# Optimization experiments

Measured on AMD Instinct MI355X. Metric: run time of the kernel, lower is better.

## Reference

```python
import jax, jax.numpy as jnp
import numpy as np

N, E, H, NH, RBF_K = 512, 4096, 128, 8, 64
CUTOFF = 10.0
HH = H * NH  # 1024


def setup_inputs() -> dict:
    key = jax.random.key(0)
    ks = jax.random.split(key, 30)
    def lin_w(k, fan_in, fan_out):
        return jax.random.normal(k, (fan_in, fan_out), jnp.float32) * (fan_in ** -0.5)
    inp = {
        'atom_embs': jax.random.normal(ks[0], (N, H), jnp.float32),
        'pos': jax.random.normal(ks[1], (N, 3), jnp.float32),
        'edge_weight': jax.random.normal(ks[2], (E,), jnp.float32),
        'edge_indices': jax.random.randint(ks[3], (2, E), 0, N, jnp.int64),
        'Wq': lin_w(ks[4], H, HH),
        'Wk': lin_w(ks[5], H, HH),
        'Wv': lin_w(ks[6], H, HH),
        'li_w': lin_w(ks[7], H, H), 'li_b': jnp.zeros((H,), jnp.float32),
        'lj_w': lin_w(ks[8], H, H), 'lj_b': jnp.zeros((H,), jnp.float32),
        'el_w': lin_w(ks[9], 3 * H, HH), 'el_b': jnp.zeros((HH,), jnp.float32),
        'rl_w': lin_w(ks[10], RBF_K, HH), 'rl_b': jnp.zeros((HH,), jnp.float32),
        'ol_w': lin_w(ks[11], HH, H), 'ol_b': jnp.zeros((H,), jnp.float32),
        'ln_g': jnp.ones((H,), jnp.float32), 'ln_b': jnp.zeros((H,), jnp.float32),
        'f1_w': lin_w(ks[12], H, H), 'f1_b': jnp.zeros((H,), jnp.float32),
        'f2_w': lin_w(ks[13], H, H), 'f2_b': jnp.zeros((H,), jnp.float32),
        'f3_w': lin_w(ks[14], H, H), 'f3_b': jnp.zeros((H,), jnp.float32),
    }
    return inp


def _scatter_softmax_cols(logits, seg, num_segments):
    # softmax over columns of `logits` grouped by seg (column -> source node)
    lt = logits.T                                   # [E_cols, E_rows]
    m = jax.ops.segment_max(lt, seg, num_segments=num_segments)
    e = jnp.exp(lt - m[seg])
    s = jax.ops.segment_sum(e, seg, num_segments=num_segments)
    return (e / s[seg]).T


def _rbf(d):
    # d: [E, 1]. ExponentialRBF with softplus(softplus_inverse(x)) == x identities
    centers = jnp.linspace(1.0, np.exp(-CUTOFF).astype(np.float32), RBF_K)
    widths = np.float32((0.5 / ((1.0 - np.exp(-CUTOFF)) / RBF_K)) ** 2)
    x = d / CUTOFF
    x3 = x ** 3; x4 = x3 * x; x5 = x4 * x
    cut = jnp.where(x < 1, 1 - 6 * x5 + 15 * x4 - 10 * x3, jnp.zeros_like(x))
    return cut * jnp.exp(-widths * (jnp.exp(-d) - centers) ** 2)   # [E, K]


def reference(atom_embs, pos, edge_weight, edge_indices, Wq, Wk, Wv,
              li_w, li_b, lj_w, lj_b, el_w, el_b, rl_w, rl_b, ol_w, ol_b,
              ln_g, ln_b, f1_w, f1_b, f2_w, f2_b, f3_w, f3_b):
    src, tgt = edge_indices[0], edge_indices[1]
    ew = edge_weight[:, None]
    ai = atom_embs[tgt] + ew                      # atom_embs_i (+= edge_weight)
    aj = atom_embs[src] + ew                      # atom_embs_j (+= edge_weight)
    Q = ai @ Wq
    K = ai @ Wk
    V = ai @ Wv                                   # [E, HH]
    logits = (Q @ K.T) * (H ** -0.5)              # [E, E]
    prod = _scatter_softmax_cols(logits, src, N)  # scatter_softmax over edge_indices[0]
    hi = ai @ li_w + li_b
    hj = aj @ lj_w + lj_b
    edge_ij = jnp.concatenate([hi + hj, hi - hj, hi * hj], axis=-1)  # [E, 3H]
    d = jnp.linalg.norm(pos[tgt] - pos[src], axis=-1)[:, None]       # [E, 1]
    feats = edge_ij @ el_w + el_b + _rbf(d) @ rl_w + rl_b + V        # [E, HH]
    msg = (prod @ feats) @ ol_w + ol_b            # [E, H]
    agg = jax.ops.segment_sum(msg, tgt, num_segments=N)              # [N, H]

    def ln(x):
        mu = jnp.mean(x, -1, keepdims=True)
        var = jnp.var(x, -1, keepdims=True)
        return (x - mu) / jnp.sqrt(var + 1e-5) * ln_g + ln_b

    h = ln(agg)
    sp = jax.nn.softplus
    h = sp(sp(sp(h @ f1_w + f1_b) @ f2_w + f2_b) @ f3_w + f3_b)
    return ln(h)
```

## Files before the change

kernel.cpp:

```cpp
#include <hip/hip_runtime.h>
#include <math.h>

#define N_NODES 512
#define NE      4096
#define H       128
#define HH      1024
#define RBFK    64
#define KCAT    576

typedef __attribute__((ext_vector_type(8))) short bf16x8;
typedef __attribute__((ext_vector_type(4))) float f32x4;
typedef __attribute__((ext_vector_type(4))) short short4v;

__device__ __forceinline__ short f2bf(float x) {
    unsigned u = __builtin_bit_cast(unsigned, x);
    unsigned r = u + 0x7FFFu + ((u >> 16) & 1u);
    return (short)(r >> 16);
}
__device__ __forceinline__ float bf2f(short s) {
    return __builtin_bit_cast(float, ((unsigned)(unsigned short)s) << 16);
}

__device__ __forceinline__ void gload16(const short* g, short* l) {
    __builtin_amdgcn_global_load_lds(
        (const __attribute__((address_space(1))) void*)g,
        (__attribute__((address_space(3))) void*)l, 16, 0, 0);
}


__global__ __launch_bounds__(512) void k_scan(
    const int* __restrict__ ei,
    int* __restrict__ srcG, int* __restrict__ tgtG,
    int* __restrict__ segStart, int* __restrict__ segStartT,
    int* __restrict__ cursorS, int* __restrict__ cursorT, int* __restrict__ nsegp,
    float* __restrict__ cvec)
{
    __shared__ int hS[N_NODES], hT[N_NODES], sS[N_NODES], sT[N_NODES];
    __shared__ int flag;
    int t = threadIdx.x;
    if (t == 0) {
        int any = 0;
        for (int i = 1; i < 128; i += 2) any |= ei[i];
        flag = (any == 0);
    }
    hS[t] = 0; hT[t] = 0;
    if (t < H) cvec[t] = 0.0f;
    __syncthreads();
    int is64 = flag;
    for (int e = t; e < NE; e += 512) {
        int s = is64 ? ei[2 * e]          : ei[e];
        int g = is64 ? ei[2 * NE + 2 * e] : ei[NE + e];
        srcG[e] = s; tgtG[e] = g;
        atomicAdd(&hS[s], 1);
        atomicAdd(&hT[g], 1);
    }
    __syncthreads();
    int cs = hS[t], ct = hT[t];
    sS[t] = cs; sT[t] = ct;
    __syncthreads();
    for (int off = 1; off < N_NODES; off <<= 1) {
        int a = (t >= off) ? sS[t - off] : 0;
        int b = (t >= off) ? sT[t - off] : 0;
        __syncthreads();
        sS[t] += a; sT[t] += b;
        __syncthreads();
    }
    segStart[t + 1]  = sS[t];
    segStartT[t + 1] = sT[t];
    if (t == 0) { segStart[0] = 0; segStartT[0] = 0; }
    cursorS[t] = sS[t] - cs;
    cursorT[t] = sT[t] - ct;
    hS[t] = (cs > 0) ? 1 : 0;
    __syncthreads();
    for (int off = 256; off > 0; off >>= 1) {
        if (t < off) hS[t] += hS[t + off];
        __syncthreads();
    }
    if (t == 0) nsegp[0] = hS[0];
}

__global__ void k_scatter(const int* __restrict__ src, const int* __restrict__ tgt,
                          const float* __restrict__ ew,
                          int* __restrict__ cursorS, int* __restrict__ cursorT,
                          int* __restrict__ srcS, int* __restrict__ tgtS,
                          float* __restrict__ ewS, int* __restrict__ idxT) {
    int e = blockIdx.x * blockDim.x + threadIdx.x;
    if (e < NE) {
        int s = src[e], g = tgt[e];
        int p = atomicAdd(&cursorS[s], 1);
        srcS[p] = s; tgtS[p] = g; ewS[p] = ew[e];
        int q = atomicAdd(&cursorT[g], 1);
        idxT[q] = p;
    }
}

#define RA 524288
#define RB 589824
#define RBZ 65536
#define RQ 131072
#define RK 131072
#define RD 131072
#define RE 32768
#define RG 65536
#define RF 4096
#define RTOT (RA+RB+RBZ+RQ+RK+RD+RE+RG+RF)

__global__ void k_prep_all(
    const float* __restrict__ atom_embs, const float* __restrict__ pos,
    const int* __restrict__ srcS, const int* __restrict__ tgtS, const float* __restrict__ ewS,
    const float* __restrict__ Wq, const float* __restrict__ Wk, const float* __restrict__ Wv,
    const float* __restrict__ li_w, const float* __restrict__ lj_w,
    const float* __restrict__ el_w, const float* __restrict__ rl_w,
    const float* __restrict__ ol_w, const float* __restrict__ el_b, const float* __restrict__ rl_b,
    short* __restrict__ Acat, short* __restrict__ ajB, short* __restrict__ BcatT,
    short* __restrict__ WqB, short* __restrict__ WkB, short* __restrict__ olT,
    short* __restrict__ liT, short* __restrict__ ljT, short* __restrict__ embB,
    float* __restrict__ cvec)
{
    int idx = blockIdx.x * blockDim.x + threadIdx.x;
    if (idx < RA) {
        int p = idx >> 7, h = idx & 127;
        int s = srcS[p], t = tgtS[p];
        float ew = ewS[p];
        Acat[(size_t)p * KCAT + h] = f2bf(atom_embs[t * H + h] + ew);
        ajB[idx] = f2bf(atom_embs[s * H + h] + ew);
        if (h < RBFK) {
            float dx = pos[t * 3 + 0] - pos[s * 3 + 0];
            float dy = pos[t * 3 + 1] - pos[s * 3 + 1];
            float dz = pos[t * 3 + 2] - pos[s * 3 + 2];
            float d = sqrtf(dx * dx + dy * dy + dz * dz);
            float x = d * 0.1f;
            float cut = 0.0f;
            if (x < 1.0f) {
                float x3 = x * x * x, x4 = x3 * x, x5 = x4 * x;
                cut = 1.0f - 6.0f * x5 + 15.0f * x4 - 10.0f * x3;
            }
            float ck = 1.0f + (float)h * (-0.015872295239210119f);
            float tt = expf(-d) - ck;
            Acat[(size_t)p * KCAT + 512 + h] = f2bf(cut * expf(-1024.0929857f * tt * tt));
        }
        return;
    }
    idx -= RA;
    if (idx < RB) {
        int k = idx >> 10, n = idx & 1023;
        float v = (k < 128) ? Wv[k * HH + n]
                : (k < 512) ? el_w[(k - 128) * HH + n]
                            : rl_w[(k - 512) * HH + n];
        BcatT[idx] = f2bf(v);
        return;
    }
    idx -= RB;
    if (idx < RBZ) { BcatT[RB + idx] = 0; return; }
    idx -= RBZ;
    if (idx < RQ) { WqB[idx] = f2bf(Wq[idx]); return; }
    idx -= RQ;
    if (idx < RK) { WkB[idx] = f2bf(Wk[idx]); return; }
    idx -= RK;
    if (idx < RD) {
        int h = idx >> 10, n = idx & 1023;
        olT[idx] = f2bf(ol_w[n * H + h]);
        return;
    }
    idx -= RD;
    if (idx < RE) {
        int which = idx >> 14, r = idx & 16383;
        int n = r >> 7, k = r & 127;
        (which ? ljT : liT)[r] = f2bf((which ? lj_w : li_w)[k * H + n]);
        return;
    }
    idx -= RE;
    if (idx < RG) { embB[idx] = f2bf(atom_embs[idx]); return; }
    idx -= RG;
    if (idx < RF) {
        int h = idx & 127, chunk = idx >> 7;
        float acc = 0.0f;
        int n0 = chunk * 32;
        for (int n = n0; n < n0 + 32; n++)
            acc += (el_b[n] + rl_b[n]) * ol_w[n * H + h];
        atomicAdd(&cvec[h], acc);
    }
}

__device__ __forceinline__ void gemm_body(
    short* As, short* Bs,
    const short* __restrict__ A, int lda,
    const short* __restrict__ B, int ldb,
    void* __restrict__ Cp, int ldc,
    int kbeg, int kend, float alpha, const float* __restrict__ bias,
    long zoff_pitch, int out_mode, int row0, int col0)
{
    const int tid = threadIdx.x;
    const int wave = tid >> 6, lane = tid & 63;

    f32x4 acc[4][4];
#pragma unroll
    for (int i = 0; i < 4; i++)
#pragma unroll
        for (int j = 0; j < 4; j++) acc[i][j] = (f32x4){0.f, 0.f, 0.f, 0.f};

    const int m0 = (wave >> 1) * 64, n0 = (wave & 1) * 64;
    const int lr = lane >> 3;
    const int lc = (lane & 7) * 8;
    const int cl = lane & 15, quad = lane >> 4;

    for (int k0 = kbeg; k0 < kend; k0 += 64) {
#pragma unroll
        for (int i = 0; i < 4; i++) {
            int r = wave * 32 + i * 8;
            gload16(A + (size_t)(row0 + r + lr) * lda + k0 + lc, As + r * 64);
            gload16(B + (size_t)(col0 + r + lr) * ldb + k0 + lc, Bs + r * 64);
        }
        __syncthreads();
#pragma unroll
        for (int kk = 0; kk < 64; kk += 32) {
            bf16x8 af[4], bf[4];
            int ko = kk + quad * 8;
#pragma unroll
            for (int i = 0; i < 4; i++)
                af[i] = *(const bf16x8*)(As + (m0 + i * 16 + cl) * 64 + ko);
#pragma unroll
            for (int j = 0; j < 4; j++)
                bf[j] = *(const bf16x8*)(Bs + (n0 + j * 16 + cl) * 64 + ko);
#pragma unroll
            for (int i = 0; i < 4; i++)
#pragma unroll
                for (int j = 0; j < 4; j++)
                    acc[i][j] = __builtin_amdgcn_mfma_f32_16x16x32_bf16(af[i], bf[j], acc[i][j], 0, 0, 0);
        }
        __syncthreads();
    }

    if (out_mode == 1) {
        short* C = (short*)Cp;
#pragma unroll
        for (int i = 0; i < 4; i++)
#pragma unroll
            for (int j = 0; j < 4; j++) {
                int cc = col0 + n0 + j * 16 + cl;
                float bv = bias ? bias[cc] : 0.0f;
#pragma unroll
                for (int reg = 0; reg < 4; reg++) {
                    int rr = row0 + m0 + i * 16 + quad * 4 + reg;
                    C[(size_t)rr * ldc + cc] = f2bf(acc[i][j][reg] * alpha + bv);
                }
            }
    } else if (out_mode == 3) {
        short* C = (short*)Cp;
#pragma unroll
        for (int i = 0; i < 4; i++)
#pragma unroll
            for (int j = 0; j < 4; j++) {
                int cc = col0 + n0 + j * 16 + cl;
                int rr = row0 + m0 + i * 16 + quad * 4;
                short4v pack;
#pragma unroll
                for (int reg = 0; reg < 4; reg++) pack[reg] = f2bf(acc[i][j][reg] * alpha);
                *(short4v*)(C + (size_t)cc * ldc + rr) = pack;
            }
    } else {
        float* C = (float*)Cp + zoff_pitch;
#pragma unroll
        for (int i = 0; i < 4; i++)
#pragma unroll
            for (int j = 0; j < 4; j++) {
                int cc = col0 + n0 + j * 16 + cl;
#pragma unroll
                for (int reg = 0; reg < 4; reg++) {
                    int rr = row0 + m0 + i * 16 + quad * 4 + reg;
                    C[(size_t)rr * ldc + cc] = acc[i][j][reg] * alpha;
                }
            }
    }
}

__global__ __launch_bounds__(256) void k_gemm(
    const short* __restrict__ A, int lda,
    const short* __restrict__ B, int ldb,
    void* __restrict__ Cp, int ldc,
    int K, float alpha, const float* __restrict__ bias,
    long split_pitch, int out_mode)
{
    __shared__ __align__(16) short As[128 * 64];
    __shared__ __align__(16) short Bs[128 * 64];
    int kchunk = K / gridDim.z;
    gemm_body(As, Bs, A, lda, B, ldb, Cp, ldc,
              kchunk * blockIdx.z, kchunk * (blockIdx.z + 1), alpha, bias,
              (long)blockIdx.z * split_pitch, out_mode,
              blockIdx.y * 128, blockIdx.x * 128);
}

__global__ __launch_bounds__(256) void k_smallgemms(
    const short* __restrict__ olT, const short* __restrict__ BcatT,
    const short* __restrict__ WqB, const short* __restrict__ WkB,
    short* __restrict__ W2T, short* __restrict__ MT)
{
    __shared__ __align__(16) short As[128 * 64];
    __shared__ __align__(16) short Bs[128 * 64];
    if (blockIdx.x < 5) {
        gemm_body(As, Bs, olT, HH, BcatT, HH, W2T, 640, 0, HH, 1.0f, nullptr, 0, 1,
                  0, blockIdx.x * 128);
    } else {
        gemm_body(As, Bs, WqB, HH, WkB, HH, MT, 128, 0, HH, 1.0f, nullptr, 0, 3, 0, 0);
    }
}

__global__ __launch_bounds__(256) void k_midgemms(
    const short* __restrict__ Acat, const short* __restrict__ W2T,
    const short* __restrict__ MT, const short* __restrict__ embB,
    short* __restrict__ GT, short* __restrict__ Y)
{
    __shared__ __align__(16) short As[128 * 64];
    __shared__ __align__(16) short Bs[128 * 64];
    if (blockIdx.x < 32) {
        gemm_body(As, Bs, Acat, KCAT, W2T, 640, GT, NE, 0, KCAT, 1.0f, nullptr, 0, 3,
                  blockIdx.x * 128, 0);
    } else {
        gemm_body(As, Bs, embB, H, MT, H, Y, H, 0, H, 1.0f, nullptr, 0, 1,
                  (blockIdx.x - 32) * 128, 0);
    }
}

__global__ __launch_bounds__(256) void k_zgemm(
    const short* __restrict__ Y, const short* __restrict__ embB,
    const short* __restrict__ MT, const int* __restrict__ tgtS,
    const float* __restrict__ ewS,
    float* __restrict__ Z, float* __restrict__ pv,
    float* __restrict__ colP, float* __restrict__ colB)
{
    const float alpha = 0.08838834764831845f;
    __shared__ __align__(16) short As[128 * 64];
    __shared__ __align__(16) short Bs[128 * 64];
    if (blockIdx.x < 16) {
        gemm_body(As, Bs, Y, H, embB, H, Z, N_NODES, 0, H, alpha, nullptr, 0, 0,
                  (blockIdx.x >> 2) * 128, (blockIdx.x & 3) * 128);
    } else {
        __shared__ float csM[H];
        __shared__ float qsh[N_NODES];
        __shared__ float sSh;
        int t = threadIdx.x;
        if (t < H) {
            float a = 0.0f;
            for (int i = 0; i < H; i++) a += bf2f(MT[t * H + i]);
            csM[t] = a;
        }
        __syncthreads();
        for (int n = t; n < N_NODES; n += 256) {
            float a = 0.0f, b = 0.0f;
            for (int k = 0; k < H; k++) {
                a += bf2f(Y[n * H + k]);
                b += csM[k] * bf2f(embB[n * H + k]);
            }
            pv[n] = a; qsh[n] = b;
        }
        if (t == 0) {
            float s = 0.0f;
            for (int k = 0; k < H; k++) s += csM[k];
            sSh = s;
        }
        __syncthreads();
        float s = sSh;
        for (int c = t; c < NE; c += 256) {
            float ec = ewS[c];
            colP[c] = alpha * ec;
            colB[c] = alpha * (qsh[tgtS[c]] + ec * s);
        }
    }
}

__global__ __launch_bounds__(256) void k_edgefeat(
    const short* __restrict__ Acat_in, const short* __restrict__ ajB,
    const short* __restrict__ liT, const short* __restrict__ ljT,
    const float* __restrict__ li_b, const float* __restrict__ lj_b,
    short* __restrict__ Acat)
{
    __shared__ __align__(16) short As[128 * 128];
    __shared__ __align__(16) short Bs[128 * 128];
    const int tid = threadIdx.x;
    const int wave = tid >> 6, lane = tid & 63;
    const int row0 = blockIdx.x * 128;
    const int cl = lane & 15, quad = lane >> 4;
    const int m0 = (wave >> 1) * 64, n0 = (wave & 1) * 64;
    const int sr = lane >> 4, sc = (lane & 15) * 8;

    f32x4 ai_acc[4][4], aj_acc[4][4];
#pragma unroll
    for (int i = 0; i < 4; i++)
#pragma unroll
        for (int j = 0; j < 4; j++) {
            ai_acc[i][j] = (f32x4){0.f, 0.f, 0.f, 0.f};
            aj_acc[i][j] = (f32x4){0.f, 0.f, 0.f, 0.f};
        }

#pragma unroll
    for (int i = 0; i < 8; i++) {
        int r = wave * 32 + i * 4;
        gload16(Acat_in + (size_t)(row0 + r + sr) * KCAT + sc, As + r * 128);
        gload16(liT + (r + sr) * 128 + sc, Bs + r * 128);
    }
    __syncthreads();
#pragma unroll
    for (int kk = 0; kk < 128; kk += 32) {
        bf16x8 af[4], bf[4];
        int ko = kk + quad * 8;
#pragma unroll
        for (int i = 0; i < 4; i++) af[i] = *(const bf16x8*)(As + (m0 + i * 16 + cl) * 128 + ko);
#pragma unroll
        for (int j = 0; j < 4; j++) bf[j] = *(const bf16x8*)(Bs + (n0 + j * 16 + cl) * 128 + ko);
#pragma unroll
        for (int i = 0; i < 4; i++)
#pragma unroll
            for (int j = 0; j < 4; j++)
                ai_acc[i][j] = __builtin_amdgcn_mfma_f32_16x16x32_bf16(af[i], bf[j], ai_acc[i][j], 0, 0, 0);
    }
    __syncthreads();
#pragma unroll
    for (int i = 0; i < 8; i++) {
        int r = wave * 32 + i * 4;
        gload16(ajB + (size_t)(row0 + r + sr) * 128 + sc, As + r * 128);
        gload16(ljT + (r + sr) * 128 + sc, Bs + r * 128);
    }
    __syncthreads();
#pragma unroll
    for (int kk = 0; kk < 128; kk += 32) {
        bf16x8 af[4], bf[4];
        int ko = kk + quad * 8;
#pragma unroll
        for (int i = 0; i < 4; i++) af[i] = *(const bf16x8*)(As + (m0 + i * 16 + cl) * 128 + ko);
#pragma unroll
        for (int j = 0; j < 4; j++) bf[j] = *(const bf16x8*)(Bs + (n0 + j * 16 + cl) * 128 + ko);
#pragma unroll
        for (int i = 0; i < 4; i++)
#pragma unroll
            for (int j = 0; j < 4; j++)
                aj_acc[i][j] = __builtin_amdgcn_mfma_f32_16x16x32_bf16(af[i], bf[j], aj_acc[i][j], 0, 0, 0);
    }
#pragma unroll
    for (int i = 0; i < 4; i++)
#pragma unroll
        for (int j = 0; j < 4; j++) {
            int cc = n0 + j * 16 + cl;
            float bi = li_b[cc], bj = lj_b[cc];
#pragma unroll
            for (int reg = 0; reg < 4; reg++) {
                int rr = row0 + m0 + i * 16 + quad * 4 + reg;
                float hv = ai_acc[i][j][reg] + bi;
                float gv = aj_acc[i][j][reg] + bj;
                short* rowp = Acat + (size_t)rr * KCAT;
                rowp[128 + cc] = f2bf(hv + gv);
                rowp[256 + cc] = f2bf(hv - gv);
                rowp[384 + cc] = f2bf(hv * gv);
            }
        }
}

__global__ __launch_bounds__(256) void k_softmax_z(
    const float* __restrict__ Z, const float* __restrict__ pv,
    const float* __restrict__ colP, const float* __restrict__ colB,
    const int* __restrict__ tgtS, const float* __restrict__ ewS,
    const int* __restrict__ srcS, const int* __restrict__ segStart,
    short* __restrict__ P)
{
    __shared__ float row[NE];
    __shared__ float zrow[N_NODES];
    __shared__ float rD[N_NODES];
    const int r = blockIdx.x, t = threadIdx.x;
    const int tr = tgtS[r];
    const float er = ewS[r];
    for (int i = t; i < N_NODES; i += 256)
        zrow[i] = Z[(size_t)tr * N_NODES + i];
    __syncthreads();
    const float p_tr = pv[tr];
    for (int c = t; c < NE; c += 256)
        row[c] = __expf(zrow[tgtS[c]] + colP[c] * p_tr + er * colB[c]);
    __syncthreads();
    for (int n = t; n < N_NODES; n += 256) {
        int a = segStart[n], b = segStart[n + 1];
        float s = 0.0f;
        for (int p = a; p < b; p++) s += row[p];
        rD[n] = (s > 0.0f) ? 1.0f / s : 0.0f;
    }
    __syncthreads();
    short* pr = P + (size_t)r * NE;
    for (int c = 2 * t; c < NE; c += 512) {
        unsigned lo = (unsigned short)f2bf(row[c] * rD[srcS[c]]);
        unsigned hi = (unsigned short)f2bf(row[c + 1] * rD[srcS[c + 1]]);
        *(unsigned*)(pr + c) = lo | (hi << 16);
    }
}

__global__ __launch_bounds__(128) void k_head(
    const float* __restrict__ msgP, const int* __restrict__ idxT,
    const int* __restrict__ segStartT, const int* __restrict__ nsegp,
    const float* __restrict__ cvec, const float* __restrict__ ol_b,
    const float* __restrict__ ln_g, const float* __restrict__ ln_b,
    const float* __restrict__ f1_w, const float* __restrict__ f1_b,
    const float* __restrict__ f2_w, const float* __restrict__ f2_b,
    const float* __restrict__ f3_w, const float* __restrict__ f3_b,
    float* __restrict__ out)
{
    __shared__ float x[H];
    __shared__ float red[H];
    int t = threadIdx.x, row = blockIdx.x;
    int a = segStartT[row], b = segStartT[row + 1];
    float v = (float)(b - a) * (ol_b[t] + (float)nsegp[0] * cvec[t]);
    for (int p = a; p < b; p++) {
        int e = idxT[p];
        const float* mp = msgP + (size_t)e * H + t;
#pragma unroll
        for (int z = 0; z < 4; z++) v += mp[(size_t)z * NE * H];
    }
    red[t] = v; __syncthreads();
    for (int s = 64; s > 0; s >>= 1) { if (t < s) red[t] += red[t + s]; __syncthreads(); }
    float mu = red[0] * (1.0f / H); __syncthreads();
    float dv = v - mu;
    red[t] = dv * dv; __syncthreads();
    for (int s = 64; s > 0; s >>= 1) { if (t < s) red[t] += red[t + s]; __syncthreads(); }
    float var = red[0] * (1.0f / H); __syncthreads();
    x[t] = dv * rsqrtf(var + 1e-5f) * ln_g[t] + ln_b[t];
    __syncthreads();
    const float* Ws[3] = { f1_w, f2_w, f3_w };
    const float* Bb[3] = { f1_b, f2_b, f3_b };
    for (int l = 0; l < 3; l++) {
        float acc = Bb[l][t];
        const float* Wl = Ws[l];
        for (int k = 0; k < H; k++) acc = fmaf(x[k], Wl[k * H + t], acc);
        float o = fmaxf(acc, 0.0f) + log1pf(expf(-fabsf(acc)));
        __syncthreads();
        x[t] = o;
        __syncthreads();
    }
    float xv = x[t];
    red[t] = xv; __syncthreads();
    for (int s = 64; s > 0; s >>= 1) { if (t < s) red[t] += red[t + s]; __syncthreads(); }
    mu = red[0] * (1.0f / H); __syncthreads();
    float dv2 = xv - mu;
    red[t] = dv2 * dv2; __syncthreads();
    for (int s = 64; s > 0; s >>= 1) { if (t < s) red[t] += red[t + s]; __syncthreads(); }
    var = red[0] * (1.0f / H);
    out[row * H + t] = dv2 * rsqrtf(var + 1e-5f) * ln_g[t] + ln_b[t];
}


extern "C" void kernel_launch(void* const* d_in, const int* in_sizes, int n_in,
                              void* d_out, int out_size, void* d_ws, size_t ws_size,
                              hipStream_t stream) {
    const float* atom_embs   = (const float*)d_in[0];
    const float* pos         = (const float*)d_in[1];
    const float* edge_weight = (const float*)d_in[2];
    const int*   edge_idx    = (const int*)d_in[3];
    const float* Wq   = (const float*)d_in[4];
    const float* Wk   = (const float*)d_in[5];
    const float* Wv   = (const float*)d_in[6];
    const float* li_w = (const float*)d_in[7];
    const float* li_b = (const float*)d_in[8];
    const float* lj_w = (const float*)d_in[9];
    const float* lj_b = (const float*)d_in[10];
    const float* el_w = (const float*)d_in[11];
    const float* el_b = (const float*)d_in[12];
    const float* rl_w = (const float*)d_in[13];
    const float* rl_b = (const float*)d_in[14];
    const float* ol_w = (const float*)d_in[15];
    const float* ol_b = (const float*)d_in[16];
    const float* ln_g = (const float*)d_in[17];
    const float* ln_b = (const float*)d_in[18];
    const float* f1_w = (const float*)d_in[19];
    const float* f1_b = (const float*)d_in[20];
    const float* f2_w = (const float*)d_in[21];
    const float* f2_b = (const float*)d_in[22];
    const float* f3_w = (const float*)d_in[23];
    const float* f3_b = (const float*)d_in[24];
    float* out = (float*)d_out;

    char* w = (char*)d_ws;
    size_t off = 0;
    auto alloc = [&](size_t bytes) -> void* {
        void* p = w + off;
        off += (bytes + 255) & ~(size_t)255;
        return p;
    };
    int*   src       = (int*)alloc(NE * 4);
    int*   tgt       = (int*)alloc(NE * 4);
    int*   srcS      = (int*)alloc(NE * 4);
    int*   tgtS      = (int*)alloc(NE * 4);
    float* ewS       = (float*)alloc(NE * 4);
    int*   segStart  = (int*)alloc((N_NODES + 1) * 4);
    int*   segStartT = (int*)alloc((N_NODES + 1) * 4);
    int*   cursorS   = (int*)alloc(N_NODES * 4);
    int*   cursorT   = (int*)alloc(N_NODES * 4);
    int*   idxT      = (int*)alloc(NE * 4);
    int*   nsegp     = (int*)alloc(4);
    short* Acat   = (short*)alloc((size_t)NE * KCAT * 2);
    short* ajB    = (short*)alloc((size_t)NE * H * 2);
    short* BcatT  = (short*)alloc((size_t)640 * HH * 2);
    short* WqB    = (short*)alloc((size_t)H * HH * 2);
    short* WkB    = (short*)alloc((size_t)H * HH * 2);
    short* olT    = (short*)alloc((size_t)H * HH * 2);
    short* liT    = (short*)alloc((size_t)H * H * 2);
    short* ljT    = (short*)alloc((size_t)H * H * 2);
    short* embB   = (short*)alloc((size_t)N_NODES * H * 2);
    float* cvec   = (float*)alloc(H * 4);
    short* W2T    = (short*)alloc((size_t)H * 640 * 2);
    short* MT     = (short*)alloc((size_t)H * H * 2);
    short* Y      = (short*)alloc((size_t)N_NODES * H * 2);
    float* Z      = (float*)alloc((size_t)N_NODES * N_NODES * 4);
    float* pv     = (float*)alloc(N_NODES * 4);
    float* colP   = (float*)alloc(NE * 4);
    float* colB   = (float*)alloc(NE * 4);
    short* GT     = (short*)alloc((size_t)H * NE * 2);
    short* prodB  = (short*)alloc((size_t)NE * NE * 2);
    float* msgP   = (float*)alloc((size_t)4 * NE * H * 4);

    k_scan<<<1, 512, 0, stream>>>(edge_idx, src, tgt, segStart, segStartT,
                                  cursorS, cursorT, nsegp, cvec);
    k_scatter<<<NE / 256, 256, 0, stream>>>(src, tgt, edge_weight, cursorS, cursorT,
                                            srcS, tgtS, ewS, idxT);
    k_prep_all<<<(RTOT + 255) / 256, 256, 0, stream>>>(
        atom_embs, pos, srcS, tgtS, ewS,
        Wq, Wk, Wv, li_w, lj_w, el_w, rl_w, ol_w, el_b, rl_b,
        Acat, ajB, BcatT, WqB, WkB, olT, liT, ljT, embB, cvec);
    k_edgefeat<<<NE / 128, 256, 0, stream>>>(Acat, ajB, liT, ljT, li_b, lj_b, Acat);

    k_smallgemms<<<6, 256, 0, stream>>>(olT, BcatT, WqB, WkB, W2T, MT);
    k_midgemms<<<36, 256, 0, stream>>>(Acat, W2T, MT, embB, GT, Y);
    k_zgemm<<<17, 256, 0, stream>>>(Y, embB, MT, tgtS, ewS, Z, pv, colP, colB);

    k_softmax_z<<<NE, 256, 0, stream>>>(Z, pv, colP, colB, tgtS, ewS, srcS, segStart, prodB);
    {
        dim3 g(1, NE / 128, 4);
        k_gemm<<<g, 256, 0, stream>>>(prodB, NE, GT, NE, msgP, H, NE, 1.0f, nullptr,
                                      (long)NE * H, 0);
    }
    k_head<<<N_NODES, H, 0, stream>>>(msgP, idxT, segStartT, nsegp, cvec, ol_b,
                                      ln_g, ln_b, f1_w, f1_b, f2_w, f2_b, f3_w, f3_b, out);
}
```

Baseline: 251.7 us.

## Fuse softmax probability generation into message GEMM, chunked by source segments

Removes the full E×E bf16 probability matrix. The softmax kernel now only writes per-row reciprocal denominators for each source segment. A new GEMM kernel rebuilds the probabilities on the fly from Z, colP/colB and those denominators while forming the A operand. Columns are split into chunks of 64 source nodes, so each block only iterates the columns of its segments, with partial sums reduced in the head kernel. This avoids a large HBM write and read. The cost is per-element exp and scattered gathers inside the GEMM loop, an extra denominator buffer, and a fixed width cap (MAXW) per chunk that silently truncates if a chunk holds too many edges.

```diff
diff --git a/kernel.cpp b/kernel.cpp
--- a/kernel.cpp
+++ b/kernel.cpp
@@ -7,6 +7,10 @@
 #define HH      1024
 #define RBFK    64
 #define KCAT    576
+#define GTLD    (NE + 128)
+#define NCHUNK  8
+#define SEGPC   64
+#define MAXW    768
 
 typedef __attribute__((ext_vector_type(8))) short bf16x8;
 typedef __attribute__((ext_vector_type(4))) float f32x4;
@@ -102,8 +106,9 @@
 #define RD 131072
 #define RE 32768
 #define RG 65536
+#define RGZ 16384
 #define RF 4096
-#define RTOT (RA+RB+RBZ+RQ+RK+RD+RE+RG+RF)
+#define RTOT (RA+RB+RBZ+RQ+RK+RD+RE+RG+RGZ+RF)
 
 __global__ void k_prep_all(
     const float* __restrict__ atom_embs, const float* __restrict__ pos,
@@ -115,7 +120,7 @@
     short* __restrict__ Acat, short* __restrict__ ajB, short* __restrict__ BcatT,
     short* __restrict__ WqB, short* __restrict__ WkB, short* __restrict__ olT,
     short* __restrict__ liT, short* __restrict__ ljT, short* __restrict__ embB,
-    float* __restrict__ cvec)
+    short* __restrict__ GT, float* __restrict__ cvec)
 {
     int idx = blockIdx.x * blockDim.x + threadIdx.x;
     if (idx < RA) {
@@ -172,6 +177,12 @@
     idx -= RE;
     if (idx < RG) { embB[idx] = f2bf(atom_embs[idx]); return; }
     idx -= RG;
+    if (idx < RGZ) {
+        int h = idx >> 7, t = idx & 127;
+        GT[(size_t)h * GTLD + NE + t] = 0;
+        return;
+    }
+    idx -= RGZ;
     if (idx < RF) {
         int h = idx & 127, chunk = idx >> 7;
         float acc = 0.0f;
@@ -274,22 +285,6 @@
     }
 }
 
-__global__ __launch_bounds__(256) void k_gemm(
-    const short* __restrict__ A, int lda,
-    const short* __restrict__ B, int ldb,
-    void* __restrict__ Cp, int ldc,
-    int K, float alpha, const float* __restrict__ bias,
-    long split_pitch, int out_mode)
-{
-    __shared__ __align__(16) short As[128 * 64];
-    __shared__ __align__(16) short Bs[128 * 64];
-    int kchunk = K / gridDim.z;
-    gemm_body(As, Bs, A, lda, B, ldb, Cp, ldc,
-              kchunk * blockIdx.z, kchunk * (blockIdx.z + 1), alpha, bias,
-              (long)blockIdx.z * split_pitch, out_mode,
-              blockIdx.y * 128, blockIdx.x * 128);
-}
-
 __global__ __launch_bounds__(256) void k_smallgemms(
     const short* __restrict__ olT, const short* __restrict__ BcatT,
     const short* __restrict__ WqB, const short* __restrict__ WkB,
@@ -313,7 +308,7 @@
     __shared__ __align__(16) short As[128 * 64];
     __shared__ __align__(16) short Bs[128 * 64];
     if (blockIdx.x < 32) {
-        gemm_body(As, Bs, Acat, KCAT, W2T, 640, GT, NE, 0, KCAT, 1.0f, nullptr, 0, 3,
+        gemm_body(As, Bs, Acat, KCAT, W2T, 640, GT, GTLD, 0, KCAT, 1.0f, nullptr, 0, 3,
                   blockIdx.x * 128, 0);
     } else {
         gemm_body(As, Bs, embB, H, MT, H, Y, H, 0, H, 1.0f, nullptr, 0, 1,
@@ -454,16 +449,14 @@
         }
 }
 
-__global__ __launch_bounds__(256) void k_softmax_z(
+__global__ __launch_bounds__(256) void k_denom(
     const float* __restrict__ Z, const float* __restrict__ pv,
     const float* __restrict__ colP, const float* __restrict__ colB,
     const int* __restrict__ tgtS, const float* __restrict__ ewS,
-    const int* __restrict__ srcS, const int* __restrict__ segStart,
-    short* __restrict__ P)
+    const int* __restrict__ segStart, float* __restrict__ rDen)
 {
     __shared__ float row[NE];
     __shared__ float zrow[N_NODES];
-    __shared__ float rD[N_NODES];
     const int r = blockIdx.x, t = threadIdx.x;
     const int tr = tgtS[r];
     const float er = ewS[r];
@@ -474,19 +467,128 @@
     for (int c = t; c < NE; c += 256)
         row[c] = __expf(zrow[tgtS[c]] + colP[c] * p_tr + er * colB[c]);
     __syncthreads();
+    float* rd = rDen + (size_t)r * N_NODES;
     for (int n = t; n < N_NODES; n += 256) {
         int a = segStart[n], b = segStart[n + 1];
         float s = 0.0f;
         for (int p = a; p < b; p++) s += row[p];
-        rD[n] = (s > 0.0f) ? 1.0f / s : 0.0f;
-    }
-    __syncthreads();
-    short* pr = P + (size_t)r * NE;
-    for (int c = 2 * t; c < NE; c += 512) {
-        unsigned lo = (unsigned short)f2bf(row[c] * rD[srcS[c]]);
-        unsigned hi = (unsigned short)f2bf(row[c + 1] * rD[srcS[c + 1]]);
-        *(unsigned*)(pr + c) = lo | (hi << 16);
-    }
+        rd[n] = (s > 0.0f) ? 1.0f / s : 0.0f;
+    }
+}
+
+__global__ __launch_bounds__(256) void k_msg(
+    const float* __restrict__ Z, const float* __restrict__ pv,
+    const float* __restrict__ colP, const float* __restrict__ colB,
+    const float* __restrict__ rDen,
+    const int* __restrict__ tgtS, const float* __restrict__ ewS,
+    const int* __restrict__ srcS, const int* __restrict__ segStart,
+    const short* __restrict__ GT, float* __restrict__ msgP)
+{
+    __shared__ float cP[MAXW], cB[MAXW];
+    __shared__ int   tcc[MAXW], sgc[MAXW];
+    __shared__ int   trOff[128];
+    __shared__ float ewrS[128], ptrS[128];
+    __shared__ __align__(16) short Bs[128 * 64];
+
+    const int tid = threadIdx.x;
+    const int bj = blockIdx.x;
+    const int r0 = blockIdx.y * 128;
+
+    const int cb = segStart[SEGPC * bj];
+    const int ce = segStart[SEGPC * bj + SEGPC];
+    const int cbase = cb & ~7;
+    int nk = (ce - cbase + 63) >> 6;
+    if (nk > MAXW / 64) nk = MAXW / 64;
+    const int wpad = nk << 6;
+
+    for (int lc = tid; lc < wpad; lc += 256) {
+        int c = cbase + lc;
+        if (c >= cb && c < ce) {
+            tcc[lc] = tgtS[c];
+            cP[lc]  = colP[c];
+            cB[lc]  = colB[c];
+            sgc[lc] = srcS[c];
+        } else sgc[lc] = -1;
+    }
+    if (tid < 128) {
+        int rr = r0 + tid;
+        int tr = tgtS[rr];
+        trOff[tid] = tr * N_NODES;
+        ewrS[tid] = ewS[rr];
+        ptrS[tid] = pv[tr];
+    }
+    __syncthreads();
+
+    const int wave = tid >> 6, lane = tid & 63;
+    const int m0 = (wave >> 1) * 64, n0 = (wave & 1) * 64;
+    const int lr = lane >> 3, lc8 = (lane & 7) * 8;
+    const int cl = lane & 15, quad = lane >> 4;
+
+    int zb4[4], rb4[4]; float pw4[4], er4[4];
+#pragma unroll
+    for (int i = 0; i < 4; i++) {
+        int m = m0 + i * 16 + cl;
+        zb4[i] = trOff[m]; pw4[i] = ptrS[m]; er4[i] = ewrS[m];
+        rb4[i] = (r0 + m) * N_NODES;
+    }
+
+    f32x4 acc[4][4];
+#pragma unroll
+    for (int i = 0; i < 4; i++)
+#pragma unroll
+        for (int j = 0; j < 4; j++) acc[i][j] = (f32x4){0.f, 0.f, 0.f, 0.f};
+
+    for (int k0 = 0; k0 < wpad; k0 += 64) {
+#pragma unroll
+        for (int i = 0; i < 4; i++) {
+            int hr = wave * 32 + i * 8;
+            gload16(GT + (size_t)(hr + lr) * GTLD + cbase + k0 + lc8, Bs + hr * 64);
+        }
+        __syncthreads();
+#pragma unroll
+        for (int kk = 0; kk < 64; kk += 32) {
+            bf16x8 bf[4];
+#pragma unroll
+            for (int j = 0; j < 4; j++)
+                bf[j] = *(const bf16x8*)(Bs + (n0 + j * 16 + cl) * 64 + kk + quad * 8);
+            bf16x8 af[4];
+#pragma unroll
+            for (int jj = 0; jj < 8; jj++) {
+                int lc = k0 + kk + quad * 8 + jj;
+                int sg = sgc[lc];
+                float cp = cP[lc], cbv = cB[lc];
+                int tc = (sg >= 0) ? tcc[lc] : 0;
+#pragma unroll
+                for (int i = 0; i < 4; i++) {
+                    float v = 0.0f;
+                    if (sg >= 0) {
+                        float l = Z[zb4[i] + tc] + cp * pw4[i] + er4[i] * cbv;
+                        v = __expf(l) * rDen[rb4[i] + sg];
+                    }
+                    af[i][jj] = f2bf(v);
+                }
+            }
+#pragma unroll
+            for (int i = 0; i < 4; i++)
+#pragma unroll
+                for (int j = 0; j < 4; j++)
+                    acc[i][j] = __builtin_amdgcn_mfma_f32_16x16x32_bf16(af[i], bf[j], acc[i][j], 0, 0, 0);
+        }
+        __syncthreads();
+    }
+
+    float* C = msgP + (size_t)bj * NE * H;
+#pragma unroll
+    for (int i = 0; i < 4; i++)
+#pragma unroll
+        for (int j = 0; j < 4; j++) {
+            int cc = n0 + j * 16 + cl;
+#pragma unroll
+            for (int reg = 0; reg < 4; reg++) {
+                int rr = r0 + m0 + i * 16 + quad * 4 + reg;
+                C[(size_t)rr * H + cc] = acc[i][j][reg];
+            }
+        }
 }
 
 __global__ __launch_bounds__(128) void k_head(
@@ -508,7 +610,7 @@
         int e = idxT[p];
         const float* mp = msgP + (size_t)e * H + t;
 #pragma unroll
-        for (int z = 0; z < 4; z++) v += mp[(size_t)z * NE * H];
+        for (int z = 0; z < NCHUNK; z++) v += mp[(size_t)z * NE * H];
     }
     red[t] = v; __syncthreads();
     for (int s = 64; s > 0; s >>= 1) { if (t < s) red[t] += red[t + s]; __syncthreads(); }
@@ -607,9 +709,9 @@
     float* pv     = (float*)alloc(N_NODES * 4);
     float* colP   = (float*)alloc(NE * 4);
     float* colB   = (float*)alloc(NE * 4);
-    short* GT     = (short*)alloc((size_t)H * NE * 2);
-    short* prodB  = (short*)alloc((size_t)NE * NE * 2);
-    float* msgP   = (float*)alloc((size_t)4 * NE * H * 4);
+    short* GT     = (short*)alloc((size_t)H * GTLD * 2);
+    float* rDen   = (float*)alloc((size_t)NE * N_NODES * 4);
+    float* msgP   = (float*)alloc((size_t)NCHUNK * NE * H * 4);
 
     k_scan<<<1, 512, 0, stream>>>(edge_idx, src, tgt, segStart, segStartT,
                                   cursorS, cursorT, nsegp, cvec);
@@ -618,18 +720,18 @@
     k_prep_all<<<(RTOT + 255) / 256, 256, 0, stream>>>(
         atom_embs, pos, srcS, tgtS, ewS,
         Wq, Wk, Wv, li_w, lj_w, el_w, rl_w, ol_w, el_b, rl_b,
-        Acat, ajB, BcatT, WqB, WkB, olT, liT, ljT, embB, cvec);
+        Acat, ajB, BcatT, WqB, WkB, olT, liT, ljT, embB, GT, cvec);
     k_edgefeat<<<NE / 128, 256, 0, stream>>>(Acat, ajB, liT, ljT, li_b, lj_b, Acat);
 
     k_smallgemms<<<6, 256, 0, stream>>>(olT, BcatT, WqB, WkB, W2T, MT);
     k_midgemms<<<36, 256, 0, stream>>>(Acat, W2T, MT, embB, GT, Y);
     k_zgemm<<<17, 256, 0, stream>>>(Y, embB, MT, tgtS, ewS, Z, pv, colP, colB);
 
-    k_softmax_z<<<NE, 256, 0, stream>>>(Z, pv, colP, colB, tgtS, ewS, srcS, segStart, prodB);
+    k_denom<<<NE, 256, 0, stream>>>(Z, pv, colP, colB, tgtS, ewS, segStart, rDen);
     {
-        dim3 g(1, NE / 128, 4);
-        k_gemm<<<g, 256, 0, stream>>>(prodB, NE, GT, NE, msgP, H, NE, 1.0f, nullptr,
-                                      (long)NE * H, 0);
+        dim3 g(NCHUNK, NE / 128);
+        k_msg<<<g, 256, 0, stream>>>(Z, pv, colP, colB, rDen, tgtS, ewS, srcS, segStart,
+                                     GT, msgP);
     }
     k_head<<<N_NODES, H, 0, stream>>>(msgP, idxT, segStartT, nsegp, cvec, ol_b,
                                       ln_g, ln_b, f1_w, f1_b, f2_w, f2_b, f3_w, f3_b, out);
```

Result: slower. 365.8 us (+45.3%).

## Aggregate softmax rows per target node before the final GEMM

Applied to the files above, without the earlier changes.

Because segment_sum over targets is linear, the softmax probability rows of all edges sharing a target node are summed in shared memory first. This yields a 512x4096 aggregated matrix instead of a 4096x4096 one, so the big GEMM runs over far fewer rows and the head kernel no longer gathers per-edge messages. The GEMM split-K is raised from 4 to 8 slices to keep enough blocks busy. The cost is that each of 512 blocks loops serially over its incoming edges, and edge counts per node are uneven, which risks load imbalance.

```diff
diff --git a/kernel.cpp b/kernel.cpp
--- a/kernel.cpp
+++ b/kernel.cpp
@@ -454,44 +454,53 @@
         }
 }
 
-__global__ __launch_bounds__(256) void k_softmax_z(
+__global__ __launch_bounds__(256) void k_pagg(
     const float* __restrict__ Z, const float* __restrict__ pv,
     const float* __restrict__ colP, const float* __restrict__ colB,
     const int* __restrict__ tgtS, const float* __restrict__ ewS,
     const int* __restrict__ srcS, const int* __restrict__ segStart,
-    short* __restrict__ P)
-{
+    const int* __restrict__ segStartT, const int* __restrict__ idxT,
+    short* __restrict__ PaggB)
+{
+    __shared__ float zrow[N_NODES];
+    __shared__ float Pacc[NE];
     __shared__ float row[NE];
-    __shared__ float zrow[N_NODES];
-    __shared__ float rD[N_NODES];
-    const int r = blockIdx.x, t = threadIdx.x;
-    const int tr = tgtS[r];
-    const float er = ewS[r];
+    __shared__ float rDe[N_NODES];
+    const int n = blockIdx.x, t = threadIdx.x;
     for (int i = t; i < N_NODES; i += 256)
-        zrow[i] = Z[(size_t)tr * N_NODES + i];
-    __syncthreads();
-    const float p_tr = pv[tr];
-    for (int c = t; c < NE; c += 256)
-        row[c] = __expf(zrow[tgtS[c]] + colP[c] * p_tr + er * colB[c]);
-    __syncthreads();
-    for (int n = t; n < N_NODES; n += 256) {
-        int a = segStart[n], b = segStart[n + 1];
-        float s = 0.0f;
-        for (int p = a; p < b; p++) s += row[p];
-        rD[n] = (s > 0.0f) ? 1.0f / s : 0.0f;
-    }
-    __syncthreads();
-    short* pr = P + (size_t)r * NE;
+        zrow[i] = Z[(size_t)n * N_NODES + i];
+    for (int c = t; c < NE; c += 256) Pacc[c] = 0.0f;
+    __syncthreads();
+    const float p_n = pv[n];
+    const int a = segStartT[n], b = segStartT[n + 1];
+    for (int ei = a; ei < b; ei++) {
+        const int e = idxT[ei];
+        const float er = ewS[e];
+        for (int c = t; c < NE; c += 256)
+            row[c] = __expf(zrow[tgtS[c]] + colP[c] * p_n + er * colB[c]);
+        __syncthreads();
+        for (int s = t; s < N_NODES; s += 256) {
+            int sa = segStart[s], sb = segStart[s + 1];
+            float sum = 0.0f;
+            for (int p = sa; p < sb; p++) sum += row[p];
+            rDe[s] = (sum > 0.0f) ? 1.0f / sum : 0.0f;
+        }
+        __syncthreads();
+        for (int c = t; c < NE; c += 256)
+            Pacc[c] += row[c] * rDe[srcS[c]];
+        __syncthreads();
+    }
+    short* pr = PaggB + (size_t)n * NE;
     for (int c = 2 * t; c < NE; c += 512) {
-        unsigned lo = (unsigned short)f2bf(row[c] * rD[srcS[c]]);
-        unsigned hi = (unsigned short)f2bf(row[c + 1] * rD[srcS[c + 1]]);
+        unsigned lo = (unsigned short)f2bf(Pacc[c]);
+        unsigned hi = (unsigned short)f2bf(Pacc[c + 1]);
         *(unsigned*)(pr + c) = lo | (hi << 16);
     }
 }
 
 __global__ __launch_bounds__(128) void k_head(
-    const float* __restrict__ msgP, const int* __restrict__ idxT,
-    const int* __restrict__ segStartT, const int* __restrict__ nsegp,
+    const float* __restrict__ aggP, const int* __restrict__ segStartT,
+    const int* __restrict__ nsegp,
     const float* __restrict__ cvec, const float* __restrict__ ol_b,
     const float* __restrict__ ln_g, const float* __restrict__ ln_b,
     const float* __restrict__ f1_w, const float* __restrict__ f1_b,
@@ -502,14 +511,11 @@
     __shared__ float x[H];
     __shared__ float red[H];
     int t = threadIdx.x, row = blockIdx.x;
-    int a = segStartT[row], b = segStartT[row + 1];
-    float v = (float)(b - a) * (ol_b[t] + (float)nsegp[0] * cvec[t]);
-    for (int p = a; p < b; p++) {
-        int e = idxT[p];
-        const float* mp = msgP + (size_t)e * H + t;
-#pragma unroll
-        for (int z = 0; z < 4; z++) v += mp[(size_t)z * NE * H];
-    }
+    int cnt = segStartT[row + 1] - segStartT[row];
+    float v = (float)cnt * (ol_b[t] + (float)nsegp[0] * cvec[t]);
+    const float* ap = aggP + (size_t)row * H + t;
+#pragma unroll
+    for (int z = 0; z < 8; z++) v += ap[(size_t)z * N_NODES * H];
     red[t] = v; __syncthreads();
     for (int s = 64; s > 0; s >>= 1) { if (t < s) red[t] += red[t + s]; __syncthreads(); }
     float mu = red[0] * (1.0f / H); __syncthreads();
@@ -608,8 +614,8 @@
     float* colP   = (float*)alloc(NE * 4);
     float* colB   = (float*)alloc(NE * 4);
     short* GT     = (short*)alloc((size_t)H * NE * 2);
-    short* prodB  = (short*)alloc((size_t)NE * NE * 2);
-    float* msgP   = (float*)alloc((size_t)4 * NE * H * 4);
+    short* PaggB  = (short*)alloc((size_t)N_NODES * NE * 2);
+    float* aggP   = (float*)alloc((size_t)8 * N_NODES * H * 4);
 
     k_scan<<<1, 512, 0, stream>>>(edge_idx, src, tgt, segStart, segStartT,
                                   cursorS, cursorT, nsegp, cvec);
@@ -625,12 +631,13 @@
     k_midgemms<<<36, 256, 0, stream>>>(Acat, W2T, MT, embB, GT, Y);
     k_zgemm<<<17, 256, 0, stream>>>(Y, embB, MT, tgtS, ewS, Z, pv, colP, colB);
 
-    k_softmax_z<<<NE, 256, 0, stream>>>(Z, pv, colP, colB, tgtS, ewS, srcS, segStart, prodB);
+    k_pagg<<<N_NODES, 256, 0, stream>>>(Z, pv, colP, colB, tgtS, ewS, srcS,
+                                        segStart, segStartT, idxT, PaggB);
     {
-        dim3 g(1, NE / 128, 4);
-        k_gemm<<<g, 256, 0, stream>>>(prodB, NE, GT, NE, msgP, H, NE, 1.0f, nullptr,
-                                      (long)NE * H, 0);
-    }
-    k_head<<<N_NODES, H, 0, stream>>>(msgP, idxT, segStartT, nsegp, cvec, ol_b,
-                                      ln_g, ln_b, f1_w, f1_b, f2_w, f2_b, f3_w, f3_b, out);
-}
+        dim3 g(1, N_NODES / 128, 8);
+        k_gemm<<<g, 256, 0, stream>>>(PaggB, NE, GT, NE, aggP, H, NE, 1.0f, nullptr,
+                                      (long)N_NODES * H, 0);
+    }
+    k_head<<<N_NODES, 128, 0, stream>>>(aggP, segStartT, nsegp, cvec, ol_b,
+                                        ln_g, ln_b, f1_w, f1_b, f2_w, f2_b, f3_w, f3_b, out);
+}
```

Result: slower. 300.8 us (+19.5%).
